# Performance work log

Measured on AMD Instinct MI355X. Metric: run time of the kernel, lower is better.

## Reference

```python
import jax, jax.numpy as jnp
import numpy as np

T, B, D = 4096, 8, 256  # tgt_len, batch, embed dim
P, O = 256, 256         # proj_dim, out_dim


def setup_inputs() -> dict:
    key = jax.random.key(0)
    k1, k2, k3, k4, k5 = jax.random.split(key, 5)
    return {
        "query": jax.random.normal(k1, (T, B, D), dtype=jnp.float32),
        "W_kqv": jax.random.normal(k2, (D, 3 * P), dtype=jnp.float32) * (D ** -0.5),
        "b_kqv": jax.random.normal(k3, (3 * P,), dtype=jnp.float32) * 0.02,
        "W_out": jax.random.normal(k4, (P, O), dtype=jnp.float32) * (P ** -0.5),
        "b_out": jax.random.normal(k5, (O,), dtype=jnp.float32) * 0.02,
    }


def reference(query, W_kqv, b_kqv, W_out, b_out):
    # query: [T, B, D] (Time x Batch x Channel)
    p = W_kqv.shape[1] // 3
    scaling = p ** -0.5
    qkv = query @ W_kqv + b_kqv                      # [T, B, 3P]
    q, k, v = jnp.split(qkv, 3, axis=-1)             # each [T, B, P]
    q = (q * scaling).transpose(1, 0, 2)             # [B, T, P]
    k = k.transpose(1, 0, 2)                         # [B, S, P] (S == T)
    v = v.transpose(1, 0, 2)                         # [B, S, P]
    scores = jnp.einsum('btp,bsp->bts', q, k)        # [B, T, S]
    probs = jax.nn.softmax(scores.astype(jnp.float32), axis=-1).astype(q.dtype)
    attn = jnp.einsum('bts,bsp->btp', probs, v)      # [B, T, P]
    attn = attn.transpose(1, 0, 2)                   # [T, B, P]
    return attn @ W_out + b_out                      # [T, B, O]
```

## Files before the change

kernel.cpp:

```cpp
#include <hip/hip_runtime.h>
#include <hip/hip_bf16.h>

#define T_LEN 4096
#define BATCH 8
#define D_DIM 256
#define P_DIM 256
#define O_DIM 256
#define N3    768

typedef __bf16 bf16;
typedef __attribute__((ext_vector_type(8))) __bf16 bf16x8;
typedef __attribute__((ext_vector_type(4))) __bf16 bf16x4;
typedef __attribute__((ext_vector_type(4))) float f32x4;
typedef __attribute__((ext_vector_type(16))) float f32x16;

#define MFMA16(a, b, c) __builtin_amdgcn_mfma_f32_16x16x32_bf16(a, b, c, 0, 0, 0)
#define MFMA32(a, b, c) __builtin_amdgcn_mfma_f32_32x32x16_bf16(a, b, c, 0, 0, 0)

#define LDS_P 72

#define BARRIER_LGKM() __asm__ __volatile__("s_waitcnt lgkmcnt(0)\n\ts_barrier" ::: "memory")
#define BARRIER_VM(N) __asm__ __volatile__("s_waitcnt vmcnt(" #N ")\n\ts_barrier" ::: "memory")

typedef __attribute__((address_space(1))) const unsigned int g_u32;
typedef __attribute__((address_space(3))) unsigned int l_u32;
#define GLD16(gp, lp) __builtin_amdgcn_global_load_lds((g_u32*)(gp), (l_u32*)(lp), 16, 0, 0)

__device__ __forceinline__ void wpack_body(
    const float* __restrict__ src, bf16* __restrict__ dst, int ncols, int g)
{
    const int lane = g & 63;
    const int idx = g >> 6;
    const int nt = idx & 3, kt = (idx >> 2) & 7, ch = idx >> 5;
    const int n = ch * 64 + nt * 16 + (lane & 15);
    const int kb = kt * 32 + (lane >> 4) * 8;
    bf16x8 pk;
    #pragma unroll
    for (int j = 0; j < 8; ++j) pk[j] = (bf16)src[(size_t)(kb + j) * ncols + n];
    *(bf16x8*)&dst[(size_t)g * 8] = pk;
}

__global__ __launch_bounds__(256) void wpack_all_kernel(
    const float* __restrict__ W_kqv, const float* __restrict__ W_out,
    bf16* __restrict__ wkp, bf16* __restrict__ wop)
{
    const int bid = blockIdx.x;
    if (bid < 96) {
        wpack_body(W_kqv, wkp, N3, bid * 256 + threadIdx.x);
    } else {
        wpack_body(W_out, wop, O_DIM, (bid - 96) * 256 + threadIdx.x);
    }
}

__global__ __launch_bounds__(256) void qkv_proj_kernel(
    const float* __restrict__ query, const bf16* __restrict__ wkp,
    const float* __restrict__ b_kqv,
    bf16* __restrict__ qb, bf16* __restrict__ kpk, bf16* __restrict__ vpk)
{
    __shared__ __align__(16) bf16 Tt[64][72];
    __shared__ __align__(16) bf16 Wb[2][16384];
    const int m0 = blockIdx.x * 64;
    const int t0g = m0 >> 3;
    const int tid = threadIdx.x;
    const int lane = tid & 63, wave = tid >> 6, l15 = lane & 15, quad = lane >> 4;
    const int arow = wave * 16 + l15;

#define STAGE_W(CH, NB)                                                       \
    {                                                                         \
        const bf16* gsrc = wkp + (size_t)(CH) * 16384;                        \
        _Pragma("unroll")                                                     \
        for (int j = 0; j < 8; ++j)                                           \
            GLD16(gsrc + ((size_t)j * 256 + tid) * 8,                         \
                  &Wb[NB][(j * 256 + wave * 64) * 8]);                        \
    }

    STAGE_W(0, 0);

    bf16x8 af[8];
    {
        const float* qsrc = query + (size_t)(m0 + arow) * D_DIM + quad * 8;
        #pragma unroll
        for (int kt = 0; kt < 8; ++kt) {
            float4 f0 = *(const float4*)(qsrc + kt * 32);
            float4 f1 = *(const float4*)(qsrc + kt * 32 + 4);
            af[kt] = bf16x8{(bf16)f0.x, (bf16)f0.y, (bf16)f0.z, (bf16)f0.w,
                            (bf16)f1.x, (bf16)f1.y, (bf16)f1.z, (bf16)f1.w};
        }
    }

    for (int ch = 0; ch < 12; ++ch) {
        const int buf = ch & 1;
        if (ch < 11) {
            STAGE_W(ch + 1, buf ^ 1);
            BARRIER_VM(8);
        } else {
            BARRIER_VM(0);
        }

        f32x4 acc[4];
        #pragma unroll
        for (int i = 0; i < 4; ++i)
            for (int r = 0; r < 4; ++r) acc[i][r] = 0.f;
        #pragma unroll
        for (int kt = 0; kt < 8; ++kt) {
            #pragma unroll
            for (int nt = 0; nt < 4; ++nt) {
                bf16x8 bb = *(const bf16x8*)&Wb[buf][((kt * 4 + nt) * 64 + lane) * 8];
                acc[nt] = MFMA16(af[kt], bb, acc[nt]);
            }
        }

        BARRIER_LGKM();

        if (ch < 8) {
            const float scale = (ch < 4) ? 0.0625f : 1.0f;
            #pragma unroll
            for (int nt = 0; nt < 4; ++nt) {
                const int c = ch * 64 + nt * 16 + l15;
                const float bias = b_kqv[c];
                #pragma unroll
                for (int r = 0; r < 4; ++r)
                    Tt[wave * 16 + quad * 4 + r][nt * 16 + l15]
                        = (bf16)((acc[nt][r] + bias) * scale);
            }
            BARRIER_LGKM();
            if (ch < 4) {
                #pragma unroll
                for (int uu = 0; uu < 2; ++uu) {
                    const int u = tid * 2 + uu;
                    const int row = u >> 3, cl = u & 7;
                    bf16x8 pk = *(const bf16x8*)&Tt[row][cl * 8];
                    const int m = m0 + row, t = m >> 3, bi = m & 7;
                    *(bf16x8*)&qb[((size_t)bi * T_LEN + t) * P_DIM + ch * 64 + cl * 8] = pk;
                }
            } else {
                #pragma unroll
                for (int uu = 0; uu < 2; ++uu) {
                    const int u = tid * 2 + uu;
                    const int cl = u >> 6, bi = (u >> 3) & 7, idx = u & 7;
                    const int row = idx * 8 + bi;
                    bf16x8 pk = *(const bf16x8*)&Tt[row][cl * 8];
                    const int t = t0g + idx;
                    const int st32 = t >> 5, n31 = t & 31;
                    const int c16 = (ch - 4) * 4 + (cl >> 1), halfk = cl & 1;
                    *(bf16x8*)&kpk[(size_t)((((bi * 128 + st32) * 16 + c16) * 64
                                             + halfk * 32 + n31) * 8)] = pk;
                }
            }
        } else {
            #pragma unroll
            for (int nt = 0; nt < 4; ++nt) {
                const int c = ch * 64 + nt * 16 + l15;
                const float bias = b_kqv[c];
                #pragma unroll
                for (int r = 0; r < 4; ++r)
                    Tt[nt * 16 + l15][wave * 16 + quad * 4 + r] = (bf16)(acc[nt][r] + bias);
            }
            BARRIER_LGKM();
            const int s64 = t0g >> 6, ks = (t0g >> 4) & 3, halfv = (t0g >> 3) & 1;
            #pragma unroll
            for (int uu = 0; uu < 2; ++uu) {
                const int u = tid * 2 + uu;
                const int cl = u >> 3, bi = u & 7;
                bf16x8 pk;
                #pragma unroll
                for (int j = 0; j < 8; ++j) pk[j] = Tt[cl][j * 8 + bi];
                const int cc = (ch - 8) * 64 + cl;
                const int ptG = cc >> 5, n31 = cc & 31;
                *(bf16x8*)&vpk[((((size_t)bi * 64 + s64) * 4 + ks) * 8 + ptG) * 512
                               + (size_t)(halfv * 32 + n31) * 8] = pk;
            }
        }
    }
#undef STAGE_W
}

__global__ __launch_bounds__(256, 2) void flash_attn_kernel(
    const bf16* __restrict__ qb, const bf16* __restrict__ kpk,
    const bf16* __restrict__ vpk, const bf16* __restrict__ wop,
    const float* __restrict__ b_out, float* __restrict__ out)
{
    __shared__ __align__(16) bf16 Ps[2][64][LDS_P];
    __shared__ float l_red[2][64];
    __shared__ __align__(16) bf16 At[64][264];

    const int bid = blockIdx.x;
    const int b = bid & 7;
    const int t0 = (bid >> 3) * 64;
    const int tid = threadIdx.x;
    const int lane = tid & 63, wave = tid >> 6;
    const int l31 = lane & 31, half = lane >> 5;
    const int rg = wave & 1, sh = wave >> 1;

    bf16x8 qf[16];
    {
        const bf16* qrow = qb + ((size_t)b * T_LEN + t0 + rg * 32 + l31) * P_DIM + half * 8;
        #pragma unroll
        for (int kt = 0; kt < 16; ++kt) qf[kt] = *(const bf16x8*)(qrow + kt * 16);
    }

    f32x16 acc_o[2][2];
    float l_part[16];
    #pragma unroll
    for (int i = 0; i < 16; ++i) {
        acc_o[0][0][i] = 0.f; acc_o[0][1][i] = 0.f;
        acc_o[1][0][i] = 0.f; acc_o[1][1][i] = 0.f;
        l_part[i] = 0.f;
    }

    const bf16* kfb = kpk + (size_t)b * 128 * 16 * 512;
    const bf16* vfb = vpk + (size_t)b * 64 * 4 * 8 * 512;

    bf16x8 kpre[8];
    {
        const bf16* kf0 = kfb + ((size_t)sh * 16 * 64 + lane) * 8;
        #pragma unroll
        for (int c = 0; c < 8; ++c) kpre[c] = *(const bf16x8*)(kf0 + (size_t)c * 512);
    }

    for (int s0 = 0; s0 < T_LEN; s0 += 64) {
        const int buf = (s0 >> 6) & 1;
        const bf16* kf  = kfb + (((size_t)((s0 >> 5) + sh)) * 16 * 64 + lane) * 8;
        const bf16* kfn = kfb + (((size_t)(((s0 + 64) >> 5) + sh)) * 16 * 64 + lane) * 8;

        bf16x8 kc2[8];
        #pragma unroll
        for (int c = 0; c < 8; ++c) kc2[c] = *(const bf16x8*)(kf + (size_t)(8 + c) * 512);

        f32x16 accsA, accsB;
        #pragma unroll
        for (int i = 0; i < 16; ++i) { accsA[i] = 0.f; accsB[i] = 0.f; }
        #pragma unroll
        for (int c = 0; c < 8; ++c) {
            accsA = MFMA32(qf[c],     kpre[c], accsA);
            accsB = MFMA32(qf[8 + c], kc2[c],  accsB);
        }
        f32x16 accs;
        #pragma unroll
        for (int i = 0; i < 16; ++i) accs[i] = accsA[i] + accsB[i];

        const bf16* vf = vfb + (((size_t)(s0 >> 6) * 4) * 8 + wave * 2) * 512 + (size_t)lane * 8;
        bf16x8 bv[8];
        #pragma unroll
        for (int ks = 0; ks < 4; ++ks) {
            bv[ks * 2]     = *(const bf16x8*)(vf + (size_t)ks * 8 * 512);
            bv[ks * 2 + 1] = *(const bf16x8*)(vf + (size_t)(ks * 8 + 1) * 512);
        }
        #pragma unroll
        for (int c = 0; c < 8; ++c) kpre[c] = *(const bf16x8*)(kfn + (size_t)c * 512);

        #pragma unroll
        for (int r = 0; r < 16; ++r) {
            float p = __expf(accs[r]);
            bf16 pb = (bf16)p;
            l_part[r] += (float)pb;
            int row = rg * 32 + (r & 3) + 8 * (r >> 2) + 4 * half;
            Ps[buf][row][sh * 32 + l31] = pb;
        }

        BARRIER_LGKM();

        #pragma unroll
        for (int ks = 0; ks < 4; ++ks) {
            bf16x8 ap0 = *(const bf16x8*)&Ps[buf][l31][ks * 16 + half * 8];
            bf16x8 ap1 = *(const bf16x8*)&Ps[buf][32 + l31][ks * 16 + half * 8];
            acc_o[0][0] = MFMA32(ap0, bv[ks * 2],     acc_o[0][0]);
            acc_o[0][1] = MFMA32(ap0, bv[ks * 2 + 1], acc_o[0][1]);
            acc_o[1][0] = MFMA32(ap1, bv[ks * 2],     acc_o[1][0]);
            acc_o[1][1] = MFMA32(ap1, bv[ks * 2 + 1], acc_o[1][1]);
        }
    }

    #pragma unroll
    for (int r = 0; r < 16; ++r) {
        float v = l_part[r];
        v += __shfl_xor(v, 1, 64);
        v += __shfl_xor(v, 2, 64);
        v += __shfl_xor(v, 4, 64);
        v += __shfl_xor(v, 8, 64);
        v += __shfl_xor(v, 16, 64);
        l_part[r] = v;
    }
    if (l31 == 0) {
        #pragma unroll
        for (int r = 0; r < 16; ++r) {
            const int row = rg * 32 + (r & 3) + 8 * (r >> 2) + 4 * half;
            l_red[sh][row] = l_part[r];
        }
    }
    __syncthreads();

    #pragma unroll
    for (int rt = 0; rt < 2; ++rt) {
        #pragma unroll
        for (int r = 0; r < 16; ++r) {
            const int row = rt * 32 + (r & 3) + 8 * (r >> 2) + 4 * half;
            const float linv = 1.0f / (l_red[0][row] + l_red[1][row]);
            At[row][wave * 64 + l31]      = (bf16)(acc_o[rt][0][r] * linv);
            At[row][wave * 64 + 32 + l31] = (bf16)(acc_o[rt][1][r] * linv);
        }
    }
    __syncthreads();

    {
        const int l15 = lane & 15, quad = lane >> 4;
        const int arow = wave * 16 + l15;
        bf16x8 af[8];
        #pragma unroll
        for (int kt = 0; kt < 8; ++kt)
            af[kt] = *(const bf16x8*)&At[arow][quad * 8 + kt * 32];

        for (int ch = 0; ch < 4; ++ch) {
            f32x4 acc[4];
            #pragma unroll
            for (int i = 0; i < 4; ++i)
                for (int r = 0; r < 4; ++r) acc[i][r] = 0.f;
            #pragma unroll
            for (int kt = 0; kt < 8; ++kt) {
                #pragma unroll
                for (int nt = 0; nt < 4; ++nt) {
                    bf16x8 bb = *(const bf16x8*)&wop[((((size_t)ch * 8 + kt) * 4 + nt) * 64 + lane) * 8];
                    acc[nt] = MFMA16(af[kt], bb, acc[nt]);
                }
            }
            #pragma unroll
            for (int nt = 0; nt < 4; ++nt) {
                const int n = ch * 64 + nt * 16 + l15;
                const float bias = b_out[n];
                #pragma unroll
                for (int r = 0; r < 4; ++r) {
                    const int t = t0 + wave * 16 + quad * 4 + r;
                    out[((size_t)t * BATCH + b) * O_DIM + n] = acc[nt][r] + bias;
                }
            }
        }
    }
}

extern "C" void kernel_launch(void* const* d_in, const int* in_sizes, int n_in,
                              void* d_out, int out_size, void* d_ws, size_t ws_size,
                              hipStream_t stream) {
    const float* query = (const float*)d_in[0];
    const float* W_kqv = (const float*)d_in[1];
    const float* b_kqv = (const float*)d_in[2];
    const float* W_out = (const float*)d_in[3];
    const float* b_out = (const float*)d_in[4];
    float* out = (float*)d_out;

    const size_t BUF = (size_t)BATCH * T_LEN * P_DIM;
    bf16* qb   = (bf16*)d_ws;
    bf16* kpk  = qb + BUF;
    bf16* vpk  = kpk + BUF;
    bf16* scr  = vpk + BUF;
    bf16* wkp  = scr;
    bf16* wop  = scr + 262144;

    wpack_all_kernel<<<128, 256, 0, stream>>>(W_kqv, W_out, wkp, wop);
    qkv_proj_kernel<<<512, 256, 0, stream>>>(query, wkp, b_kqv, qb, kpk, vpk);
    flash_attn_kernel<<<512, 256, 0, stream>>>(qb, kpk, vpk, wop, b_out, out);
}
```

Before: 267.8 us.

## Fuse weight pack, QKV projection and attention into one cooperative kernel

Merges the three launches into a single cooperative kernel that uses grid-wide syncs between the weight-packing, QKV-projection and flash-attention phases, sharing one LDS buffer across phases. This is meant to remove launch gaps and inter-kernel drain/fill overhead. It forces 512 blocks to be co-resident at 74.7KB LDS each, which may be rejected (falling back to three launches) and caps occupancy of the attention phase at the larger LDS footprint.

```diff
diff --git a/kernel.cpp b/kernel.cpp
--- a/kernel.cpp
+++ b/kernel.cpp
@@ -1,5 +1,8 @@
 #include <hip/hip_runtime.h>
 #include <hip/hip_bf16.h>
+#include <hip/hip_cooperative_groups.h>
+
+namespace cg = cooperative_groups;
 
 #define T_LEN 4096
 #define BATCH 8
@@ -10,7 +13,6 @@
 
 typedef __bf16 bf16;
 typedef __attribute__((ext_vector_type(8))) __bf16 bf16x8;
-typedef __attribute__((ext_vector_type(4))) __bf16 bf16x4;
 typedef __attribute__((ext_vector_type(4))) float f32x4;
 typedef __attribute__((ext_vector_type(16))) float f32x16;
 
@@ -40,26 +42,13 @@
     *(bf16x8*)&dst[(size_t)g * 8] = pk;
 }
 
-__global__ __launch_bounds__(256) void wpack_all_kernel(
-    const float* __restrict__ W_kqv, const float* __restrict__ W_out,
-    bf16* __restrict__ wkp, bf16* __restrict__ wop)
-{
-    const int bid = blockIdx.x;
-    if (bid < 96) {
-        wpack_body(W_kqv, wkp, N3, bid * 256 + threadIdx.x);
-    } else {
-        wpack_body(W_out, wop, O_DIM, (bid - 96) * 256 + threadIdx.x);
-    }
-}
-
-__global__ __launch_bounds__(256) void qkv_proj_kernel(
+__device__ __forceinline__ void qkv_body(
     const float* __restrict__ query, const bf16* __restrict__ wkp,
     const float* __restrict__ b_kqv,
-    bf16* __restrict__ qb, bf16* __restrict__ kpk, bf16* __restrict__ vpk)
-{
-    __shared__ __align__(16) bf16 Tt[64][72];
-    __shared__ __align__(16) bf16 Wb[2][16384];
-    const int m0 = blockIdx.x * 64;
+    bf16* __restrict__ qb, bf16* __restrict__ kpk, bf16* __restrict__ vpk,
+    bf16* Tt, bf16* Wb, int bidx)
+{
+    const int m0 = bidx * 64;
     const int t0g = m0 >> 3;
     const int tid = threadIdx.x;
     const int lane = tid & 63, wave = tid >> 6, l15 = lane & 15, quad = lane >> 4;
@@ -71,7 +60,7 @@
         _Pragma("unroll")                                                     \
         for (int j = 0; j < 8; ++j)                                           \
             GLD16(gsrc + ((size_t)j * 256 + tid) * 8,                         \
-                  &Wb[NB][(j * 256 + wave * 64) * 8]);                        \
+                  &Wb[(NB) * 16384 + (j * 256 + wave * 64) * 8]);             \
     }
 
     STAGE_W(0, 0);
@@ -105,7 +94,7 @@
         for (int kt = 0; kt < 8; ++kt) {
             #pragma unroll
             for (int nt = 0; nt < 4; ++nt) {
-                bf16x8 bb = *(const bf16x8*)&Wb[buf][((kt * 4 + nt) * 64 + lane) * 8];
+                bf16x8 bb = *(const bf16x8*)&Wb[buf * 16384 + ((kt * 4 + nt) * 64 + lane) * 8];
                 acc[nt] = MFMA16(af[kt], bb, acc[nt]);
             }
         }
@@ -120,7 +109,7 @@
                 const float bias = b_kqv[c];
                 #pragma unroll
                 for (int r = 0; r < 4; ++r)
-                    Tt[wave * 16 + quad * 4 + r][nt * 16 + l15]
+                    Tt[(wave * 16 + quad * 4 + r) * 72 + nt * 16 + l15]
                         = (bf16)((acc[nt][r] + bias) * scale);
             }
             BARRIER_LGKM();
@@ -129,7 +118,7 @@
                 for (int uu = 0; uu < 2; ++uu) {
                     const int u = tid * 2 + uu;
                     const int row = u >> 3, cl = u & 7;
-                    bf16x8 pk = *(const bf16x8*)&Tt[row][cl * 8];
+                    bf16x8 pk = *(const bf16x8*)&Tt[row * 72 + cl * 8];
                     const int m = m0 + row, t = m >> 3, bi = m & 7;
                     *(bf16x8*)&qb[((size_t)bi * T_LEN + t) * P_DIM + ch * 64 + cl * 8] = pk;
                 }
@@ -139,7 +128,7 @@
                     const int u = tid * 2 + uu;
                     const int cl = u >> 6, bi = (u >> 3) & 7, idx = u & 7;
                     const int row = idx * 8 + bi;
-                    bf16x8 pk = *(const bf16x8*)&Tt[row][cl * 8];
+                    bf16x8 pk = *(const bf16x8*)&Tt[row * 72 + cl * 8];
                     const int t = t0g + idx;
                     const int st32 = t >> 5, n31 = t & 31;
                     const int c16 = (ch - 4) * 4 + (cl >> 1), halfk = cl & 1;
@@ -154,7 +143,7 @@
                 const float bias = b_kqv[c];
                 #pragma unroll
                 for (int r = 0; r < 4; ++r)
-                    Tt[nt * 16 + l15][wave * 16 + quad * 4 + r] = (bf16)(acc[nt][r] + bias);
+                    Tt[(nt * 16 + l15) * 72 + wave * 16 + quad * 4 + r] = (bf16)(acc[nt][r] + bias);
             }
             BARRIER_LGKM();
             const int s64 = t0g >> 6, ks = (t0g >> 4) & 3, halfv = (t0g >> 3) & 1;
@@ -164,7 +153,7 @@
                 const int cl = u >> 3, bi = u & 7;
                 bf16x8 pk;
                 #pragma unroll
-                for (int j = 0; j < 8; ++j) pk[j] = Tt[cl][j * 8 + bi];
+                for (int j = 0; j < 8; ++j) pk[j] = Tt[cl * 72 + j * 8 + bi];
                 const int cc = (ch - 8) * 64 + cl;
                 const int ptG = cc >> 5, n31 = cc & 31;
                 *(bf16x8*)&vpk[((((size_t)bi * 64 + s64) * 4 + ks) * 8 + ptG) * 512
@@ -175,18 +164,18 @@
 #undef STAGE_W
 }
 
-__global__ __launch_bounds__(256, 2) void flash_attn_kernel(
+__device__ __forceinline__ void flash_body(
     const bf16* __restrict__ qb, const bf16* __restrict__ kpk,
     const bf16* __restrict__ vpk, const bf16* __restrict__ wop,
-    const float* __restrict__ b_out, float* __restrict__ out)
-{
-    __shared__ __align__(16) bf16 Ps[2][64][LDS_P];
-    __shared__ float l_red[2][64];
-    __shared__ __align__(16) bf16 At[64][264];
-
-    const int bid = blockIdx.x;
-    const int b = bid & 7;
-    const int t0 = (bid >> 3) * 64;
+    const float* __restrict__ b_out, float* __restrict__ out,
+    char* smem, int bidx)
+{
+    bf16*  Ps    = (bf16*)smem;
+    float* l_red = (float*)(smem + 18432);
+    bf16*  At    = (bf16*)(smem + 18944);
+
+    const int b = bidx & 7;
+    const int t0 = (bidx >> 3) * 64;
     const int tid = threadIdx.x;
     const int lane = tid & 63, wave = tid >> 6;
     const int l31 = lane & 31, half = lane >> 5;
@@ -255,15 +244,15 @@
             bf16 pb = (bf16)p;
             l_part[r] += (float)pb;
             int row = rg * 32 + (r & 3) + 8 * (r >> 2) + 4 * half;
-            Ps[buf][row][sh * 32 + l31] = pb;
+            Ps[(buf * 64 + row) * LDS_P + sh * 32 + l31] = pb;
         }
 
         BARRIER_LGKM();
 
         #pragma unroll
         for (int ks = 0; ks < 4; ++ks) {
-            bf16x8 ap0 = *(const bf16x8*)&Ps[buf][l31][ks * 16 + half * 8];
-            bf16x8 ap1 = *(const bf16x8*)&Ps[buf][32 + l31][ks * 16 + half * 8];
+            bf16x8 ap0 = *(const bf16x8*)&Ps[(buf * 64 + l31) * LDS_P + ks * 16 + half * 8];
+            bf16x8 ap1 = *(const bf16x8*)&Ps[(buf * 64 + 32 + l31) * LDS_P + ks * 16 + half * 8];
             acc_o[0][0] = MFMA32(ap0, bv[ks * 2],     acc_o[0][0]);
             acc_o[0][1] = MFMA32(ap0, bv[ks * 2 + 1], acc_o[0][1]);
             acc_o[1][0] = MFMA32(ap1, bv[ks * 2],     acc_o[1][0]);
@@ -285,7 +274,7 @@
         #pragma unroll
         for (int r = 0; r < 16; ++r) {
             const int row = rg * 32 + (r & 3) + 8 * (r >> 2) + 4 * half;
-            l_red[sh][row] = l_part[r];
+            l_red[sh * 64 + row] = l_part[r];
         }
     }
     __syncthreads();
@@ -295,9 +284,9 @@
         #pragma unroll
         for (int r = 0; r < 16; ++r) {
             const int row = rt * 32 + (r & 3) + 8 * (r >> 2) + 4 * half;
-            const float linv = 1.0f / (l_red[0][row] + l_red[1][row]);
-            At[row][wave * 64 + l31]      = (bf16)(acc_o[rt][0][r] * linv);
-            At[row][wave * 64 + 32 + l31] = (bf16)(acc_o[rt][1][r] * linv);
+            const float linv = 1.0f / (l_red[row] + l_red[64 + row]);
+            At[row * 264 + wave * 64 + l31]      = (bf16)(acc_o[rt][0][r] * linv);
+            At[row * 264 + wave * 64 + 32 + l31] = (bf16)(acc_o[rt][1][r] * linv);
         }
     }
     __syncthreads();
@@ -308,7 +297,7 @@
         bf16x8 af[8];
         #pragma unroll
         for (int kt = 0; kt < 8; ++kt)
-            af[kt] = *(const bf16x8*)&At[arow][quad * 8 + kt * 32];
+            af[kt] = *(const bf16x8*)&At[arow * 264 + quad * 8 + kt * 32];
 
         for (int ch = 0; ch < 4; ++ch) {
             f32x4 acc[4];
@@ -335,6 +324,61 @@
             }
         }
     }
+}
+
+__global__ __launch_bounds__(256) void wpack_all_kernel(
+    const float* __restrict__ W_kqv, const float* __restrict__ W_out,
+    bf16* __restrict__ wkp, bf16* __restrict__ wop)
+{
+    const int bid = blockIdx.x;
+    if (bid < 96) {
+        wpack_body(W_kqv, wkp, N3, bid * 256 + threadIdx.x);
+    } else {
+        wpack_body(W_out, wop, O_DIM, (bid - 96) * 256 + threadIdx.x);
+    }
+}
+
+__global__ __launch_bounds__(256) void qkv_proj_kernel(
+    const float* __restrict__ query, const bf16* __restrict__ wkp,
+    const float* __restrict__ b_kqv,
+    bf16* __restrict__ qb, bf16* __restrict__ kpk, bf16* __restrict__ vpk)
+{
+    __shared__ __align__(16) bf16 Tt[64 * 72];
+    __shared__ __align__(16) bf16 Wb[2 * 16384];
+    qkv_body(query, wkp, b_kqv, qb, kpk, vpk, Tt, Wb, blockIdx.x);
+}
+
+__global__ __launch_bounds__(256, 2) void flash_attn_kernel(
+    const bf16* __restrict__ qb, const bf16* __restrict__ kpk,
+    const bf16* __restrict__ vpk, const bf16* __restrict__ wop,
+    const float* __restrict__ b_out, float* __restrict__ out)
+{
+    __shared__ __align__(16) char smem[52736];
+    flash_body(qb, kpk, vpk, wop, b_out, out, smem, blockIdx.x);
+}
+
+__global__ __launch_bounds__(256, 2) void fused_all_kernel(
+    const float* __restrict__ query, const float* __restrict__ W_kqv,
+    const float* __restrict__ b_kqv, const float* __restrict__ W_out,
+    const float* __restrict__ b_out,
+    bf16* __restrict__ qb, bf16* __restrict__ kpk, bf16* __restrict__ vpk,
+    bf16* __restrict__ wkp, bf16* __restrict__ wop, float* __restrict__ out)
+{
+    cg::grid_group grid = cg::this_grid();
+    __shared__ __align__(16) char smem[74752];
+    const int bid = blockIdx.x;
+
+    if (bid < 128) {
+        if (bid < 96) wpack_body(W_kqv, wkp, N3, bid * 256 + threadIdx.x);
+        else          wpack_body(W_out, wop, O_DIM, (bid - 96) * 256 + threadIdx.x);
+    }
+    grid.sync();
+
+    qkv_body(query, wkp, b_kqv, qb, kpk, vpk,
+             (bf16*)smem, (bf16*)(smem + 9216), bid);
+    grid.sync();
+
+    flash_body(qb, kpk, vpk, wop, b_out, out, smem, bid);
 }
 
 extern "C" void kernel_launch(void* const* d_in, const int* in_sizes, int n_in,
@@ -355,7 +399,18 @@
     bf16* wkp  = scr;
     bf16* wop  = scr + 262144;
 
-    wpack_all_kernel<<<128, 256, 0, stream>>>(W_kqv, W_out, wkp, wop);
-    qkv_proj_kernel<<<512, 256, 0, stream>>>(query, wkp, b_kqv, qb, kpk, vpk);
-    flash_attn_kernel<<<512, 256, 0, stream>>>(qb, kpk, vpk, wop, b_out, out);
-}
+    void* args[] = {
+        (void*)&query, (void*)&W_kqv, (void*)&b_kqv, (void*)&W_out,
+        (void*)&b_out, (void*)&qb, (void*)&kpk, (void*)&vpk,
+        (void*)&wkp, (void*)&wop, (void*)&out
+    };
+    hipError_t err = hipLaunchCooperativeKernel(
+        reinterpret_cast<void*>(fused_all_kernel),
+        dim3(512), dim3(256), args, 0, stream);
+
+    if (err != hipSuccess) {
+        wpack_all_kernel<<<128, 256, 0, stream>>>(W_kqv, W_out, wkp, wop);
+        qkv_proj_kernel<<<512, 256, 0, stream>>>(query, wkp, b_kqv, qb, kpk, vpk);
+        flash_attn_kernel<<<512, 256, 0, stream>>>(qb, kpk, vpk, wop, b_out, out);
+    }
+}
```

Measured after the change: 391.6 us. 46.2% more time.
